# Kernel optimization log

Measured on AMD Instinct MI355X. Metric: run time of the kernel, lower is better.

The kernel has to match this reference:

```python
import jax, jax.numpy as jnp
import numpy as np

N_SUPPORT = 16384
EMBED_DIM = 1024
MAX_LEVELS = 4
N_CLASSES = 64


def setup_inputs() -> dict:
    key = jax.random.key(0)
    ks = jax.random.split(key, 12)
    D, L = EMBED_DIM, MAX_LEVELS
    s = 0.02
    return {
        "support_features": jax.random.normal(ks[0], (N_SUPPORT, D), jnp.float32),
        "support_labels": jax.random.randint(ks[1], (N_SUPPORT,), 0, N_CLASSES),
        "sp_w1": jax.random.normal(ks[2], (D, D // 2), jnp.float32) * s,
        "sp_b1": jnp.zeros((D // 2,), jnp.float32),
        "sp_w2": jax.random.normal(ks[3], (D // 2, L), jnp.float32) * s,
        "sp_b2": jnp.zeros((L,), jnp.float32),
        "lvl_emb": jax.random.normal(ks[4], (L, 1), jnp.float32) * s,
        "an_w1": jax.random.normal(ks[5], (L, D + 1, D), jnp.float32) * s,
        "an_b1": jnp.zeros((L, D), jnp.float32),
        "an_gamma": jnp.ones((L, D), jnp.float32),
        "an_beta": jnp.zeros((L, D), jnp.float32),
        "an_w2": jax.random.normal(ks[6], (L, D, D), jnp.float32) * s,
        "an_b2": jnp.zeros((L, D), jnp.float32),
        "fu_w1": jax.random.normal(ks[7], (L * D + L, D), jnp.float32) * s,
        "fu_b1": jnp.zeros((D,), jnp.float32),
        "fu_w2": jax.random.normal(ks[8], (D, D), jnp.float32) * s,
        "fu_b2": jnp.zeros((D,), jnp.float32),
        "n_classes": N_CLASSES,
    }


def _forward(support_features, support_labels, sp_w1, sp_b1, sp_w2, sp_b2,
             lvl_emb, an_w1, an_b1, an_gamma, an_beta, an_w2, an_b2,
             fu_w1, fu_b1, fu_w2, fu_b2, n_classes):
    N, D = support_features.shape
    L = an_w1.shape[0]
    # structure predictor on task context (mean pooled support set)
    task_context = support_features.mean(axis=0)
    h = jax.nn.relu(task_context @ sp_w1 + sp_b1)
    acts = jax.nn.sigmoid(h @ sp_w2 + sp_b2)  # [L]
    ones = jnp.ones((N,), support_features.dtype)
    counts = jax.ops.segment_sum(ones, support_labels, num_segments=n_classes)[:, None]
    counts = jnp.maximum(counts, 1.0)
    # per-level small MLP over ALL support points, then per-class mean via segment_sum
    protos = []
    for l in range(L):  # fixed small loop over structurally distinct level params
        xl = jnp.concatenate([support_features, jnp.broadcast_to(lvl_emb[l], (N, 1))], axis=1)  # [N, D+1]
        hh = xl @ an_w1[l] + an_b1[l]
        mu = hh.mean(axis=-1, keepdims=True)
        var = ((hh - mu) ** 2).mean(axis=-1, keepdims=True)
        hh = (hh - mu) / jnp.sqrt(var + 1e-5) * an_gamma[l] + an_beta[l]  # LayerNorm eps=1e-5
        hh = jax.nn.relu(hh)
        t = hh @ an_w2[l] + an_b2[l]
        protos.append(jax.ops.segment_sum(t, support_labels, num_segments=n_classes) / counts)
    protos = jnp.stack(protos, axis=1)  # [C, L, D]
    # data-dependent gating: pack prototypes of active levels (act > 0.1) to the front,
    # then active weights, then zero padding -- matching torch's concat+pad layout
    mask = acts > 0.1
    mi = mask.astype(jnp.int32)
    slots = jnp.cumsum(mi) - 1          # destination slot of each active level
    k = mi.sum()                        # number of active levels
    slot_or_dump = jnp.where(mask, slots, L)
    packed = jnp.zeros((n_classes, L + 1, D), protos.dtype).at[:, slot_or_dump, :].set(protos)[:, :L, :]
    S = L * D + L
    buf = jnp.zeros((n_classes, S + 1), protos.dtype)
    buf = buf.at[:, : L * D].set(packed.reshape(n_classes, L * D))
    widx = jnp.where(mask, k * D + slots, S)  # weights placed right after the k packed prototypes
    buf = buf.at[:, widx].set(jnp.broadcast_to(acts, (n_classes, L)))
    fusion_input = buf[:, :S]  # [C, L*D + L]
    fused = jax.nn.relu(fusion_input @ fu_w1 + fu_b1) @ fu_w2 + fu_b2  # [C, D]
    raw_mean = jax.ops.segment_sum(support_features, support_labels, num_segments=n_classes) / counts
    prototypes = jnp.where(k > 0, fused, raw_mean)
    level_contributions = jnp.where(mask, acts, 0.0)
    return prototypes, acts, level_contributions


def reference(support_features, support_labels, sp_w1, sp_b1, sp_w2, sp_b2,
              lvl_emb, an_w1, an_b1, an_gamma, an_beta, an_w2, an_b2,
              fu_w1, fu_b1, fu_w2, fu_b2, n_classes):
    return _forward(support_features, support_labels, sp_w1, sp_b1, sp_w2, sp_b2,
                    lvl_emb, an_w1, an_b1, an_gamma, an_beta, an_w2, an_b2,
                    fu_w1, fu_b1, fu_w2, fu_b2, n_classes)
```

## Files before the change

### kernel.cpp

```cpp
#include <hip/hip_runtime.h>
#include <hip/hip_bf16.h>
#include <stdint.h>

#define N_SUP 16384
#define DIM   1024
#define NLV   4
#define NCLS  64
#define NFUSE 4096

typedef __bf16 bf16x8 __attribute__((ext_vector_type(8)));
typedef __bf16 bf16x4 __attribute__((ext_vector_type(4)));
typedef float  f32x4  __attribute__((ext_vector_type(4)));

#define GLOAD_LDS16(g, l) \
    __builtin_amdgcn_global_load_lds((const __attribute__((address_space(1))) void*)(g), \
                                     (__attribute__((address_space(3))) void*)(l), 16, 0, 0)

__global__ __launch_bounds__(1024) void k_rowlist(const int* __restrict__ labels,
                                                  int* __restrict__ inv,
                                                  int* __restrict__ gstart,
                                                  int* __restrict__ gcnt,
                                                  float* __restrict__ counts_f) {
    __shared__ int cnt[NCLS];
    __shared__ int sstart[NCLS];
    __shared__ int cur[NCLS];
    int tid = threadIdx.x;
    if (tid < NCLS) cnt[tid] = 0;
    __syncthreads();
    for (int r = tid; r < N_SUP; r += 1024) atomicAdd(&cnt[labels[r]], 1);
    __syncthreads();
    if (tid == 0) {
        int run = 0;
        for (int c = 0; c < NCLS; ++c) { sstart[c] = run; run += cnt[c]; }
    }
    __syncthreads();
    if (tid < NCLS) {
        cur[tid] = sstart[tid];
        gstart[tid] = sstart[tid];
        gcnt[tid] = cnt[tid];
        counts_f[tid] = fmaxf((float)cnt[tid], 1.0f);
    }
    __syncthreads();
    for (int r = tid; r < N_SUP; r += 1024) {
        int pos = atomicAdd(&cur[labels[r]], 1);
        inv[r] = pos;
    }
}

__global__ __launch_bounds__(256) void k_conv_feat(const float* __restrict__ f,
                                                   const int* __restrict__ inv,
                                                   __bf16* __restrict__ o) {
    int r = blockIdx.x;
    int tid = threadIdx.x;
    int dr = inv[r];
    float4 v = *(const float4*)(f + (size_t)r * DIM + tid * 4);
    union { __bf16 b[4]; uint64_t u; } pk;
    pk.b[0] = (__bf16)v.x; pk.b[1] = (__bf16)v.y;
    pk.b[2] = (__bf16)v.z; pk.b[3] = (__bf16)v.w;
    *(uint64_t*)(o + (size_t)dr * DIM + tid * 4) = pk.u;
}

__global__ __launch_bounds__(256) void k_wt(const float* __restrict__ an_w1,
                                            __bf16* __restrict__ w1t) {
    __shared__ float tile[64][65];
    int m = blockIdx.z;
    const float* src = an_w1 + (size_t)m * 1025 * 1024;
    __bf16* dst = w1t + (size_t)m * 1024 * 1024;
    int k0 = blockIdx.x * 64, n0 = blockIdx.y * 64;
    int j = threadIdx.x & 63, i0 = threadIdx.x >> 6;
    #pragma unroll
    for (int ii = 0; ii < 16; ++ii) {
        int i = i0 + ii * 4;
        tile[i][j] = src[(size_t)(k0 + i) * 1024 + n0 + j];
    }
    __syncthreads();
    #pragma unroll
    for (int ii = 0; ii < 16; ++ii) {
        int i = i0 + ii * 4;
        dst[(size_t)(n0 + i) * 1024 + k0 + j] = (__bf16)tile[j][i];
    }
}

__global__ __launch_bounds__(256) void k_eff_b1(const float* __restrict__ an_w1,
                                                const float* __restrict__ an_b1,
                                                const float* __restrict__ lvl_emb,
                                                float* __restrict__ eff) {
    int i = blockIdx.x * 256 + threadIdx.x;
    int l = i >> 10, j = i & 1023;
    eff[i] = an_b1[i] + lvl_emb[l] * an_w1[(size_t)l * 1025 * 1024 + (size_t)1024 * 1024 + j];
}

__global__ __launch_bounds__(256) void k_gather(const __bf16* __restrict__ X,
                                                const int* __restrict__ gstart,
                                                const int* __restrict__ gcnt,
                                                float* __restrict__ outp,
                                                float* __restrict__ tcsum) {
    int c = blockIdx.x;
    int col = blockIdx.y * 256 + threadIdx.x;
    int st = gstart[c], n = gcnt[c];
    const __bf16* base = X + (size_t)st * DIM + col;
    float acc = 0.f;
    int i = 0;
    for (; i + 8 <= n; i += 8) {
        float v[8];
        #pragma unroll
        for (int j = 0; j < 8; ++j) v[j] = (float)base[(size_t)(i + j) * DIM];
        #pragma unroll
        for (int j = 0; j < 8; ++j) acc += v[j];
    }
    for (; i < n; ++i) acc += (float)base[(size_t)i * DIM];
    outp[(size_t)c * DIM + col] = acc;
    atomicAdd(&tcsum[col], acc);
}

__global__ __launch_bounds__(512) void k_gemv1(const float* __restrict__ tc,
                                               const float* __restrict__ sp_w1,
                                               float* __restrict__ hpre) {
    __shared__ float tcs[64];
    int tid = threadIdx.x;
    int kb = blockIdx.x * 64;
    if (tid < 64) tcs[tid] = tc[kb + tid] * (1.0f / N_SUP);
    __syncthreads();
    float acc = 0.f;
    #pragma unroll 8
    for (int k = 0; k < 64; ++k)
        acc += tcs[k] * sp_w1[(size_t)(kb + k) * 512 + tid];
    atomicAdd(&hpre[tid], acc);
}

__global__ __launch_bounds__(512) void k_head_fin(const float* __restrict__ hpre,
                                                  const float* __restrict__ sp_b1,
                                                  const float* __restrict__ sp_w2,
                                                  const float* __restrict__ sp_b2,
                                                  float* __restrict__ headf,
                                                  int* __restrict__ headi,
                                                  float* __restrict__ dout) {
    __shared__ float red[512];
    __shared__ float a4[4];
    int tid = threadIdx.x;
    float hv = hpre[tid] + sp_b1[tid];
    hv = hv > 0.f ? hv : 0.f;
    #pragma unroll
    for (int o = 0; o < 4; ++o) {
        red[tid] = hv * sp_w2[tid * 4 + o];
        __syncthreads();
        for (int st = 256; st > 0; st >>= 1) {
            if (tid < st) red[tid] += red[tid + st];
            __syncthreads();
        }
        if (tid == 0) a4[o] = 1.0f / (1.0f + expf(-(red[0] + sp_b2[o])));
        __syncthreads();
    }
    if (tid == 0) {
        int kk = 0;
        int lvl[4] = {-1, -1, -1, -1};
        for (int l = 0; l < 4; ++l)
            if (a4[l] > 0.1f) { lvl[kk] = l; kk++; }
        headi[0] = kk;
        for (int s = 0; s < 4; ++s) headi[1 + s] = lvl[s];
        for (int l = 0; l < 4; ++l) headf[l] = a4[l];
    }
    if (tid < 4) {
        dout[65536 + tid] = a4[tid];
        dout[65540 + tid] = a4[tid] > 0.1f ? a4[tid] : 0.f;
    }
}

__global__ __launch_bounds__(512, 2) void k_gemm256(const __bf16* __restrict__ A,
                                                    const __bf16* __restrict__ Bt,
                                                    const float* __restrict__ bias,
                                                    __bf16* __restrict__ C,
                                                    int K, int Nn, int NT) {
    __shared__ __bf16 lds[65536];
    const int tid = threadIdx.x;
    const int w   = tid >> 6;
    const int l   = tid & 63;
    const int wr  = w >> 2;
    const int wc  = w & 3;
    const int am  = l & 15;
    const int kg  = l >> 4;
    const size_t bm = (size_t)blockIdx.x * 256;
    const size_t bn = (size_t)blockIdx.y * 256;

    const int srow = w * 8 + (l >> 3);
    const int scol = ((l & 7) ^ (l >> 3)) * 8;
    const __bf16* gA[2][2]; const __bf16* gB[2][2];
    #pragma unroll
    for (int h = 0; h < 2; ++h)
        #pragma unroll
        for (int p = 0; p < 2; ++p) {
            gA[h][p] = A  + (bm + h * 128 + p * 64 + srow) * (size_t)K + scol;
            gB[h][p] = Bt + (bn + h * 128 + p * 64 + srow) * (size_t)K + scol;
        }

    f32x4 acc[8][4] = {};
    bf16x8 ax[4][2], ay[4][2], bx[2][2], by[2][2];

    #pragma unroll
    for (int h = 0; h < 2; ++h)
        #pragma unroll
        for (int p = 0; p < 2; ++p) {
            GLOAD_LDS16(gA[h][p], lds + h * 8192 + p * 4096 + w * 512);
            GLOAD_LDS16(gB[h][p], lds + 16384 + h * 8192 + p * 4096 + w * 512);
        }
    asm volatile("s_waitcnt vmcnt(0)" ::: "memory");
    __builtin_amdgcn_s_barrier();

    const int swz = (am & 7) * 8;
    const int ko0 = (kg * 8) ^ swz;
    const int ko1 = (32 + kg * 8) ^ swz;
    {
        const __bf16* pa0 = lds + wr * 8192;
        #pragma unroll
        for (int i = 0; i < 4; ++i) {
            ax[i][0] = *(const bf16x8*)(pa0 + (i * 16 + am) * 64 + ko0);
            ax[i][1] = *(const bf16x8*)(pa0 + (i * 16 + am) * 64 + ko1);
        }
    }

#define MFMAQ(qm, qn, AF, BF) \
    __builtin_amdgcn_s_setprio(1); \
    _Pragma("unroll") \
    for (int i_ = 0; i_ < 4; ++i_) \
        _Pragma("unroll") \
        for (int j_ = 0; j_ < 2; ++j_) \
            _Pragma("unroll") \
            for (int k_ = 0; k_ < 2; ++k_) \
                acc[(qm) * 4 + i_][(qn) * 2 + j_] = __builtin_amdgcn_mfma_f32_16x16x32_bf16( \
                    AF[i_][k_], BF[j_][k_], acc[(qm) * 4 + i_][(qn) * 2 + j_], 0, 0, 0); \
    __builtin_amdgcn_s_setprio(0);

    for (int t = 0; t < NT; ++t) {
        const int cb = (t & 1) * 32768;
        const int nb = cb ^ 32768;
        const int tn = (t + 1) * 64;
        const bool more = (t + 1 < NT);
        const __bf16* pa  = lds + cb + wr * 8192;
        const __bf16* pan = lds + nb + wr * 8192;
        const __bf16* pb  = lds + cb + 16384 + (wc >> 1) * 8192 + (wc & 1) * 4096;

        if (more) {
            GLOAD_LDS16(gA[0][0] + tn, lds + nb + 0 * 4096 + w * 512);
            GLOAD_LDS16(gA[1][0] + tn, lds + nb + 8192 + 0 * 4096 + w * 512);
            asm volatile("s_waitcnt vmcnt(2)" ::: "memory");
        } else {
            asm volatile("s_waitcnt vmcnt(0)" ::: "memory");
        }
        __builtin_amdgcn_s_barrier();
        #pragma unroll
        for (int j = 0; j < 2; ++j) {
            bx[j][0] = *(const bf16x8*)(pb + (j * 16 + am) * 64 + ko0);
            bx[j][1] = *(const bf16x8*)(pb + (j * 16 + am) * 64 + ko1);
        }
        ay[0][0] = *(const bf16x8*)(pa + ((4 + 0) * 16 + am) * 64 + ko0);
        ay[0][1] = *(const bf16x8*)(pa + ((4 + 0) * 16 + am) * 64 + ko1);
        MFMAQ(0, 0, ax, bx)

        if (more) {
            GLOAD_LDS16(gA[0][1] + tn, lds + nb + 1 * 4096 + w * 512);
            GLOAD_LDS16(gA[1][1] + tn, lds + nb + 8192 + 1 * 4096 + w * 512);
        }
        __builtin_amdgcn_s_barrier();
        #pragma unroll
        for (int j = 0; j < 2; ++j) {
            by[j][0] = *(const bf16x8*)(pb + ((2 + j) * 16 + am) * 64 + ko0);
            by[j][1] = *(const bf16x8*)(pb + ((2 + j) * 16 + am) * 64 + ko1);
        }
        ay[1][0] = *(const bf16x8*)(pa + ((4 + 1) * 16 + am) * 64 + ko0);
        ay[1][1] = *(const bf16x8*)(pa + ((4 + 1) * 16 + am) * 64 + ko1);
        MFMAQ(0, 1, ax, by)

        if (more) {
            GLOAD_LDS16(gB[0][0] + tn, lds + nb + 16384 + 0 * 4096 + w * 512);
            GLOAD_LDS16(gB[0][1] + tn, lds + nb + 16384 + 1 * 4096 + w * 512);
            asm volatile("s_waitcnt vmcnt(4)" ::: "memory");
        }
        __builtin_amdgcn_s_barrier();
        #pragma unroll
        for (int i = 2; i < 4; ++i) {
            ay[i][0] = *(const bf16x8*)(pa + ((4 + i) * 16 + am) * 64 + ko0);
            ay[i][1] = *(const bf16x8*)(pa + ((4 + i) * 16 + am) * 64 + ko1);
        }
        if (more) {
            #pragma unroll
            for (int i = 0; i < 2; ++i) {
                ax[i][0] = *(const bf16x8*)(pan + (i * 16 + am) * 64 + ko0);
                ax[i][1] = *(const bf16x8*)(pan + (i * 16 + am) * 64 + ko1);
            }
        }
        MFMAQ(1, 0, ay, bx)

        if (more) {
            GLOAD_LDS16(gB[1][0] + tn, lds + nb + 16384 + 8192 + 0 * 4096 + w * 512);
            GLOAD_LDS16(gB[1][1] + tn, lds + nb + 16384 + 8192 + 1 * 4096 + w * 512);
        }
        __builtin_amdgcn_s_barrier();
        if (more) {
            #pragma unroll
            for (int i = 2; i < 4; ++i) {
                ax[i][0] = *(const bf16x8*)(pan + (i * 16 + am) * 64 + ko0);
                ax[i][1] = *(const bf16x8*)(pan + (i * 16 + am) * 64 + ko1);
            }
        }
        MFMAQ(1, 1, ay, by)
    }
#undef MFMAQ

    const int rbase = kg * 4;
    #pragma unroll
    for (int m = 0; m < 8; ++m) {
        const size_t row = bm + wr * 128 + m * 16 + rbase;
        #pragma unroll
        for (int n = 0; n < 4; ++n) {
            const int col = (int)bn + wc * 64 + n * 16 + am;
            const float bv = bias[col];
            #pragma unroll
            for (int r = 0; r < 4; ++r)
                C[(row + r) * (size_t)Nn + col] = (__bf16)(acc[m][n][r] + bv);
        }
    }
}

__global__ __launch_bounds__(256) void k_gather_ln(const __bf16* __restrict__ hh,
                                                   const float* __restrict__ an_g,
                                                   const float* __restrict__ an_be,
                                                   const int* __restrict__ gstart,
                                                   const int* __restrict__ gcnt,
                                                   float* __restrict__ gsum) {
    int c = blockIdx.x, lv = blockIdx.y, z = blockIdx.z;
    int tid = threadIdx.x;
    int wv = tid >> 6, lane = tid & 63;
    int colb = lane * 16;
    float g[16], b[16];
    #pragma unroll
    for (int j = 0; j < 16; j += 4) {
        float4 gv = *(const float4*)(an_g + lv * 1024 + colb + j);
        float4 bv = *(const float4*)(an_be + lv * 1024 + colb + j);
        g[j] = gv.x; g[j + 1] = gv.y; g[j + 2] = gv.z; g[j + 3] = gv.w;
        b[j] = bv.x; b[j + 1] = bv.y; b[j + 2] = bv.z; b[j + 3] = bv.w;
    }
    int st = gstart[c], n = gcnt[c];
    float acc[16] = {};
    #pragma unroll 2
    for (int i = z * 4 + wv; i < n; i += 8) {
        const __bf16* row = hh + (size_t)(st + i) * NFUSE + lv * 1024 + colb;
        bf16x8 v0 = *(const bf16x8*)row;
        bf16x8 v1 = *(const bf16x8*)(row + 8);
        float x[16];
        #pragma unroll
        for (int j = 0; j < 8; ++j) { x[j] = (float)v0[j]; x[8 + j] = (float)v1[j]; }
        float s = 0.f, q = 0.f;
        #pragma unroll
        for (int j = 0; j < 16; ++j) { s += x[j]; q += x[j] * x[j]; }
        #pragma unroll
        for (int off = 1; off < 64; off <<= 1) {
            s += __shfl_xor(s, off);
            q += __shfl_xor(q, off);
        }
        float mu = s * (1.0f / DIM);
        float var = q * (1.0f / DIM) - mu * mu;
        float rstd = rsqrtf(var + 1e-5f);
        #pragma unroll
        for (int j = 0; j < 16; ++j) {
            float y = (x[j] - mu) * rstd * g[j] + b[j];
            acc[j] += y > 0.f ? y : 0.f;
        }
    }
    __shared__ float red[4][1024];
    #pragma unroll
    for (int j = 0; j < 16; ++j) red[wv][colb + j] = acc[j];
    __syncthreads();
    for (int col = tid; col < 1024; col += 256) {
        float v = red[0][col] + red[1][col] + red[2][col] + red[3][col];
        atomicAdd(&gsum[(size_t)c * NFUSE + lv * 1024 + col], v);
    }
}

__global__ __launch_bounds__(256) void k_build_fi(const float* __restrict__ proto_pre,
                                                  const float* __restrict__ an_b2,
                                                  const int* __restrict__ gcnt,
                                                  const float* __restrict__ counts_f,
                                                  const float* __restrict__ headf,
                                                  const int* __restrict__ headi,
                                                  float* __restrict__ fi) {
    int idx = blockIdx.x * 256 + threadIdx.x;
    if (idx >= 64 * 4160) return;
    int c = idx / 4160, col = idx % 4160;
    int kk = headi[0];
    float v = 0.f;
    if (col < kk * 1024) {
        int s = col >> 10, d = col & 1023;
        int l = headi[1 + s];
        if (gcnt[c] > 0)
            v = proto_pre[((size_t)l * NCLS + c) * DIM + d] / counts_f[c]
                + an_b2[(size_t)l * DIM + d];
    } else if (col < kk * 1024 + kk) {
        int s = col - kk * 1024;
        v = headf[headi[1 + s]];
    }
    fi[idx] = v;
}

__global__ __launch_bounds__(256) void k_fuse_gemm(const float* __restrict__ Abase, int lda, int az,
                                                   const float* __restrict__ Wbase, int wz,
                                                   float* __restrict__ outbase, int oz,
                                                   const float* __restrict__ abias,
                                                   int K) {
    const float* Afi = Abase + (size_t)blockIdx.z * az;
    const float* W   = Wbase + (size_t)blockIdx.z * wz;
    float* outp      = outbase + (size_t)blockIdx.z * oz;
    __shared__ float fi_lds[64][64];
    int tid = threadIdx.x;
    int tj = tid & 63, tg = tid >> 6;
    int jb = blockIdx.x;
    int k0 = blockIdx.y * 64;
    for (int i = tid; i < 64 * 64; i += 256) {
        int cc = i >> 6, kq = i & 63;
        float av = 0.f;
        if (k0 + kq < lda) {
            av = Afi[(size_t)cc * lda + k0 + kq];
            if (abias) {
                av += abias[k0 + kq];
                av = av > 0.f ? av : 0.f;
            }
        }
        fi_lds[cc][kq] = av;
    }
    __syncthreads();
    float acc[16] = {};
    #pragma unroll 4
    for (int kq = 0; kq < 64; ++kq) {
        int kg = k0 + kq;
        float wv = (kg < K) ? W[(size_t)kg * 1024 + jb * 64 + tj] : 0.f;
        #pragma unroll
        for (int cc = 0; cc < 16; ++cc)
            acc[cc] += fi_lds[tg * 16 + cc][kq] * wv;
    }
    #pragma unroll
    for (int cc = 0; cc < 16; ++cc)
        atomicAdd(&outp[(size_t)(tg * 16 + cc) * 1024 + jb * 64 + tj], acc[cc]);
}

__global__ __launch_bounds__(256) void k_final(const float* __restrict__ pre2,
                                               const float* __restrict__ fu_b2,
                                               const int* __restrict__ headi,
                                               const float* __restrict__ rawsum,
                                               const float* __restrict__ counts_f,
                                               float* __restrict__ dout) {
    int i = blockIdx.x * 256 + threadIdx.x;
    int c = i >> 10, j = i & 1023;
    float v;
    if (headi[0] > 0) v = pre2[i] + fu_b2[j];
    else              v = rawsum[i] / counts_f[c];
    dout[i] = v;
}

extern "C" void kernel_launch(void* const* d_in, const int* in_sizes, int n_in,
                              void* d_out, int out_size, void* d_ws, size_t ws_size,
                              hipStream_t stream) {
    (void)in_sizes; (void)n_in; (void)out_size; (void)ws_size;
    const float* feat    = (const float*)d_in[0];
    const int*   labels  = (const int*)d_in[1];
    const float* sp_w1   = (const float*)d_in[2];
    const float* sp_b1   = (const float*)d_in[3];
    const float* sp_w2   = (const float*)d_in[4];
    const float* sp_b2   = (const float*)d_in[5];
    const float* lvl_emb = (const float*)d_in[6];
    const float* an_w1   = (const float*)d_in[7];
    const float* an_b1   = (const float*)d_in[8];
    const float* an_g    = (const float*)d_in[9];
    const float* an_be   = (const float*)d_in[10];
    const float* an_w2   = (const float*)d_in[11];
    const float* an_b2   = (const float*)d_in[12];
    const float* fu_w1   = (const float*)d_in[13];
    const float* fu_b1   = (const float*)d_in[14];
    const float* fu_w2   = (const float*)d_in[15];
    const float* fu_b2   = (const float*)d_in[16];
    float* dout = (float*)d_out;

    char* p = (char*)d_ws;
    auto alloc = [&](size_t b) { char* r = p; p += (b + 255) & ~(size_t)255; return r; };
    __bf16* featb = (__bf16*)alloc((size_t)N_SUP * DIM * 2);
    __bf16* w1t   = (__bf16*)alloc((size_t)NLV * DIM * DIM * 2);
    __bf16* hh    = (__bf16*)alloc((size_t)N_SUP * NFUSE * 2);
    float*  effb1 = (float*) alloc((size_t)NLV * DIM * 4);
    float*  fi    = (float*) alloc((size_t)64 * 4160 * 4);
    float*  rawsum  = (float*)alloc((size_t)NCLS * DIM * 4);
    int*    inv     = (int*)  alloc((size_t)N_SUP * 4);
    int*    gstart  = (int*)  alloc(NCLS * 4);
    int*    gcnt    = (int*)  alloc(NCLS * 4);
    float*  counts_f= (float*)alloc(NCLS * 4);
    float*  headf   = (float*)alloc(4 * 4);
    int*    headi   = (int*)  alloc(8 * 4);
    char* z0 = p;
    float*  tc      = (float*)alloc(DIM * 4);
    float*  gsum    = (float*)alloc((size_t)NCLS * NFUSE * 4);
    float*  proto_pre = (float*)alloc((size_t)NLV * NCLS * DIM * 4);
    float*  h1pre   = (float*)alloc((size_t)NCLS * DIM * 4);
    float*  f2pre   = (float*)alloc((size_t)NCLS * DIM * 4);
    float*  hpre    = (float*)alloc(512 * 4);
    size_t zbytes = (size_t)(p - z0);
    hipMemsetAsync(z0, 0, zbytes, stream);

    k_eff_b1<<<16, 256, 0, stream>>>(an_w1, an_b1, lvl_emb, effb1);
    k_rowlist<<<1, 1024, 0, stream>>>(labels, inv, gstart, gcnt, counts_f);
    k_conv_feat<<<N_SUP, 256, 0, stream>>>(feat, inv, featb);
    k_wt<<<dim3(16, 16, 4), 256, 0, stream>>>(an_w1, w1t);
    k_gather<<<dim3(NCLS, 4), 256, 0, stream>>>(featb, gstart, gcnt, rawsum, tc);
    k_gemv1<<<16, 512, 0, stream>>>(tc, sp_w1, hpre);
    k_head_fin<<<1, 512, 0, stream>>>(hpre, sp_b1, sp_w2, sp_b2, headf, headi, dout);

    k_gemm256<<<dim3(64, 16), 512, 0, stream>>>(featb, w1t, effb1, hh, DIM, NFUSE, DIM / 64);
    k_gather_ln<<<dim3(NCLS, NLV, 2), 256, 0, stream>>>(hh, an_g, an_be, gstart, gcnt, gsum);
    k_fuse_gemm<<<dim3(16, 16, 4), 256, 0, stream>>>(gsum, NFUSE, 1024,
                                                     an_w2, 1024 * 1024,
                                                     proto_pre, NCLS * DIM, nullptr, 1024);

    k_build_fi<<<(64 * 4160) / 256, 256, 0, stream>>>(proto_pre, an_b2, gcnt, counts_f,
                                                      headf, headi, fi);
    k_fuse_gemm<<<dim3(16, 65, 1), 256, 0, stream>>>(fi, 4160, 0, fu_w1, 0,
                                                     h1pre, 0, nullptr, 4100);
    k_fuse_gemm<<<dim3(16, 16, 1), 256, 0, stream>>>(h1pre, 1024, 0, fu_w2, 0,
                                                     f2pre, 0, fu_b1, 1024);
    k_final<<<NCLS * DIM / 256, 256, 0, stream>>>(f2pre, fu_b2, headi, rawsum, counts_f, dout);
}
```

Before: 328.8 us.

## Restructure GEMM main loop into barrier-separated load/compute phases

Reorganizes the 256x256 bf16 MFMA GEMM main loop. The prologue now issues all global-to-LDS loads without a blocking wait. Each iteration waits on partial vmcnt, loads fragments from the current buffer, and brackets every MFMA quadrant with barriers, instead of prefetching next-tile A fragments across iterations. The aim is a simpler, more regular schedule that interleaves next-tile global loads with LDS reads and keeps waves in lockstep, but the extra barriers per iteration and the loss of cross-iteration register prefetch may cost latency.

New measurement: 336.2 us. 1.02x slower.

```diff
diff --git a/kernel.cpp b/kernel.cpp
--- a/kernel.cpp
+++ b/kernel.cpp
@@ -196,27 +196,18 @@
     f32x4 acc[8][4] = {};
     bf16x8 ax[4][2], ay[4][2], bx[2][2], by[2][2];
 
-    #pragma unroll
-    for (int h = 0; h < 2; ++h)
-        #pragma unroll
-        for (int p = 0; p < 2; ++p) {
-            GLOAD_LDS16(gA[h][p], lds + h * 8192 + p * 4096 + w * 512);
-            GLOAD_LDS16(gB[h][p], lds + 16384 + h * 8192 + p * 4096 + w * 512);
-        }
-    asm volatile("s_waitcnt vmcnt(0)" ::: "memory");
-    __builtin_amdgcn_s_barrier();
+    GLOAD_LDS16(gB[0][0], lds + 16384 + 0 * 4096 + w * 512);
+    GLOAD_LDS16(gB[0][1], lds + 16384 + 1 * 4096 + w * 512);
+    GLOAD_LDS16(gB[1][0], lds + 16384 + 8192 + 0 * 4096 + w * 512);
+    GLOAD_LDS16(gB[1][1], lds + 16384 + 8192 + 1 * 4096 + w * 512);
+    GLOAD_LDS16(gA[0][0], lds + 0 * 4096 + w * 512);
+    GLOAD_LDS16(gA[1][0], lds + 8192 + 0 * 4096 + w * 512);
+    GLOAD_LDS16(gA[0][1], lds + 1 * 4096 + w * 512);
+    GLOAD_LDS16(gA[1][1], lds + 8192 + 1 * 4096 + w * 512);
 
     const int swz = (am & 7) * 8;
     const int ko0 = (kg * 8) ^ swz;
     const int ko1 = (32 + kg * 8) ^ swz;
-    {
-        const __bf16* pa0 = lds + wr * 8192;
-        #pragma unroll
-        for (int i = 0; i < 4; ++i) {
-            ax[i][0] = *(const bf16x8*)(pa0 + (i * 16 + am) * 64 + ko0);
-            ax[i][1] = *(const bf16x8*)(pa0 + (i * 16 + am) * 64 + ko1);
-        }
-    }
 
 #define MFMAQ(qm, qn, AF, BF) \
     __builtin_amdgcn_s_setprio(1); \
@@ -235,74 +226,68 @@
         const int nb = cb ^ 32768;
         const int tn = (t + 1) * 64;
         const bool more = (t + 1 < NT);
-        const __bf16* pa  = lds + cb + wr * 8192;
-        const __bf16* pan = lds + nb + wr * 8192;
-        const __bf16* pb  = lds + cb + 16384 + (wc >> 1) * 8192 + (wc & 1) * 4096;
-
+        const __bf16* pa = lds + cb + wr * 8192;
+        const __bf16* pb = lds + cb + 16384 + (wc >> 1) * 8192 + (wc & 1) * 4096;
+
+        asm volatile("s_waitcnt vmcnt(2)" ::: "memory");
+        __builtin_amdgcn_s_barrier();
+        if (more) {
+            GLOAD_LDS16(gB[0][0] + tn, lds + nb + 16384 + 0 * 4096 + w * 512);
+            GLOAD_LDS16(gB[0][1] + tn, lds + nb + 16384 + 1 * 4096 + w * 512);
+        }
+        #pragma unroll
+        for (int i = 0; i < 4; ++i) {
+            ax[i][0] = *(const bf16x8*)(pa + (i * 16 + am) * 64 + ko0);
+            ax[i][1] = *(const bf16x8*)(pa + (i * 16 + am) * 64 + ko1);
+        }
+        #pragma unroll
+        for (int j = 0; j < 2; ++j) {
+            bx[j][0] = *(const bf16x8*)(pb + (j * 16 + am) * 64 + ko0);
+            bx[j][1] = *(const bf16x8*)(pb + (j * 16 + am) * 64 + ko1);
+        }
+        __builtin_amdgcn_s_barrier();
+        MFMAQ(0, 0, ax, bx)
+        __builtin_amdgcn_s_barrier();
+
+        if (more) {
+            GLOAD_LDS16(gB[1][0] + tn, lds + nb + 16384 + 8192 + 0 * 4096 + w * 512);
+            GLOAD_LDS16(gB[1][1] + tn, lds + nb + 16384 + 8192 + 1 * 4096 + w * 512);
+        }
+        #pragma unroll
+        for (int j = 0; j < 2; ++j) {
+            by[j][0] = *(const bf16x8*)(pb + ((2 + j) * 16 + am) * 64 + ko0);
+            by[j][1] = *(const bf16x8*)(pb + ((2 + j) * 16 + am) * 64 + ko1);
+        }
+        __builtin_amdgcn_s_barrier();
+        MFMAQ(0, 1, ax, by)
+        __builtin_amdgcn_s_barrier();
+
+        if (more) {
+            asm volatile("s_waitcnt vmcnt(4)" ::: "memory");
+        } else {
+            asm volatile("s_waitcnt vmcnt(0)" ::: "memory");
+        }
+        __builtin_amdgcn_s_barrier();
         if (more) {
             GLOAD_LDS16(gA[0][0] + tn, lds + nb + 0 * 4096 + w * 512);
             GLOAD_LDS16(gA[1][0] + tn, lds + nb + 8192 + 0 * 4096 + w * 512);
-            asm volatile("s_waitcnt vmcnt(2)" ::: "memory");
-        } else {
-            asm volatile("s_waitcnt vmcnt(0)" ::: "memory");
-        }
-        __builtin_amdgcn_s_barrier();
-        #pragma unroll
-        for (int j = 0; j < 2; ++j) {
-            bx[j][0] = *(const bf16x8*)(pb + (j * 16 + am) * 64 + ko0);
-            bx[j][1] = *(const bf16x8*)(pb + (j * 16 + am) * 64 + ko1);
-        }
-        ay[0][0] = *(const bf16x8*)(pa + ((4 + 0) * 16 + am) * 64 + ko0);
-        ay[0][1] = *(const bf16x8*)(pa + ((4 + 0) * 16 + am) * 64 + ko1);
-        MFMAQ(0, 0, ax, bx)
+        }
+        #pragma unroll
+        for (int i = 0; i < 4; ++i) {
+            ay[i][0] = *(const bf16x8*)(pa + ((4 + i) * 16 + am) * 64 + ko0);
+            ay[i][1] = *(const bf16x8*)(pa + ((4 + i) * 16 + am) * 64 + ko1);
+        }
+        __builtin_amdgcn_s_barrier();
+        MFMAQ(1, 0, ay, bx)
+        __builtin_amdgcn_s_barrier();
 
         if (more) {
             GLOAD_LDS16(gA[0][1] + tn, lds + nb + 1 * 4096 + w * 512);
             GLOAD_LDS16(gA[1][1] + tn, lds + nb + 8192 + 1 * 4096 + w * 512);
         }
         __builtin_amdgcn_s_barrier();
-        #pragma unroll
-        for (int j = 0; j < 2; ++j) {
-            by[j][0] = *(const bf16x8*)(pb + ((2 + j) * 16 + am) * 64 + ko0);
-            by[j][1] = *(const bf16x8*)(pb + ((2 + j) * 16 + am) * 64 + ko1);
-        }
-        ay[1][0] = *(const bf16x8*)(pa + ((4 + 1) * 16 + am) * 64 + ko0);
-        ay[1][1] = *(const bf16x8*)(pa + ((4 + 1) * 16 + am) * 64 + ko1);
-        MFMAQ(0, 1, ax, by)
-
-        if (more) {
-            GLOAD_LDS16(gB[0][0] + tn, lds + nb + 16384 + 0 * 4096 + w * 512);
-            GLOAD_LDS16(gB[0][1] + tn, lds + nb + 16384 + 1 * 4096 + w * 512);
-            asm volatile("s_waitcnt vmcnt(4)" ::: "memory");
-        }
-        __builtin_amdgcn_s_barrier();
-        #pragma unroll
-        for (int i = 2; i < 4; ++i) {
-            ay[i][0] = *(const bf16x8*)(pa + ((4 + i) * 16 + am) * 64 + ko0);
-            ay[i][1] = *(const bf16x8*)(pa + ((4 + i) * 16 + am) * 64 + ko1);
-        }
-        if (more) {
-            #pragma unroll
-            for (int i = 0; i < 2; ++i) {
-                ax[i][0] = *(const bf16x8*)(pan + (i * 16 + am) * 64 + ko0);
-                ax[i][1] = *(const bf16x8*)(pan + (i * 16 + am) * 64 + ko1);
-            }
-        }
-        MFMAQ(1, 0, ay, bx)
-
-        if (more) {
-            GLOAD_LDS16(gB[1][0] + tn, lds + nb + 16384 + 8192 + 0 * 4096 + w * 512);
-            GLOAD_LDS16(gB[1][1] + tn, lds + nb + 16384 + 8192 + 1 * 4096 + w * 512);
-        }
-        __builtin_amdgcn_s_barrier();
-        if (more) {
-            #pragma unroll
-            for (int i = 2; i < 4; ++i) {
-                ax[i][0] = *(const bf16x8*)(pan + (i * 16 + am) * 64 + ko0);
-                ax[i][1] = *(const bf16x8*)(pan + (i * 16 + am) * 64 + ko1);
-            }
-        }
         MFMAQ(1, 1, ay, by)
+        __builtin_amdgcn_s_barrier();
     }
 #undef MFMAQ
 
```

## Stage GEMM epilogue through LDS for 16-byte stores and swizzle block order

Applied to the files above, without the earlier changes.

The GEMM epilogue now writes accumulators into LDS one half-tile at a time, then reads them back row-contiguously so each thread emits 16-byte bf16x8 global stores with vectorized bias loads. This replaces scattered 2-byte stores. Block indices are also remapped with a hard-coded swizzle (64 x-blocks by 16 y-blocks) to improve L2 reuse across concurrently running blocks. The swizzle assumes a specific grid shape and the staging adds barriers, so it fails for other launch shapes.

After: 332.1 us. Within noise of the previous version (+1.0%).

```diff
diff --git a/kernel.cpp b/kernel.cpp
--- a/kernel.cpp
+++ b/kernel.cpp
@@ -179,8 +179,13 @@
     const int wc  = w & 3;
     const int am  = l & 15;
     const int kg  = l >> 4;
-    const size_t bm = (size_t)blockIdx.x * 256;
-    const size_t bn = (size_t)blockIdx.y * 256;
+
+    const int lin = blockIdx.y * 64 + blockIdx.x;
+    const int swz = (lin & 7) * 128 + (lin >> 3);
+    const int bxi = swz >> 4;
+    const int byi = swz & 15;
+    const size_t bm = (size_t)bxi * 256;
+    const size_t bn = (size_t)byi * 256;
 
     const int srow = w * 8 + (l >> 3);
     const int scol = ((l & 7) ^ (l >> 3)) * 8;
@@ -206,9 +211,9 @@
     asm volatile("s_waitcnt vmcnt(0)" ::: "memory");
     __builtin_amdgcn_s_barrier();
 
-    const int swz = (am & 7) * 8;
-    const int ko0 = (kg * 8) ^ swz;
-    const int ko1 = (32 + kg * 8) ^ swz;
+    const int swzr = (am & 7) * 8;
+    const int ko0 = (kg * 8) ^ swzr;
+    const int ko1 = (32 + kg * 8) ^ swzr;
     {
         const __bf16* pa0 = lds + wr * 8192;
         #pragma unroll
@@ -306,17 +311,39 @@
     }
 #undef MFMAQ
 
+    float* fl = (float*)lds;
+    const int ecol = (tid & 31) * 8;
+    float4 bia0 = *(const float4*)(bias + bn + ecol);
+    float4 bia1 = *(const float4*)(bias + bn + ecol + 4);
     const int rbase = kg * 4;
     #pragma unroll
-    for (int m = 0; m < 8; ++m) {
-        const size_t row = bm + wr * 128 + m * 16 + rbase;
-        #pragma unroll
-        for (int n = 0; n < 4; ++n) {
-            const int col = (int)bn + wc * 64 + n * 16 + am;
-            const float bv = bias[col];
+    for (int h = 0; h < 2; ++h) {
+        __syncthreads();
+        if (wr == h) {
             #pragma unroll
-            for (int r = 0; r < 4; ++r)
-                C[(row + r) * (size_t)Nn + col] = (__bf16)(acc[m][n][r] + bv);
+            for (int m = 0; m < 8; ++m) {
+                const int lr = m * 16 + rbase;
+                #pragma unroll
+                for (int n = 0; n < 4; ++n) {
+                    const int cc = wc * 64 + n * 16 + am;
+                    #pragma unroll
+                    for (int r = 0; r < 4; ++r)
+                        fl[(lr + r) * 256 + cc] = acc[m][n][r];
+                }
+            }
+        }
+        __syncthreads();
+        #pragma unroll
+        for (int it = 0; it < 8; ++it) {
+            const int row = (tid >> 5) + it * 16;
+            f32x4 v0 = *(const f32x4*)(fl + row * 256 + ecol);
+            f32x4 v1 = *(const f32x4*)(fl + row * 256 + ecol + 4);
+            bf16x8 ov;
+            ov[0] = (__bf16)(v0[0] + bia0.x); ov[1] = (__bf16)(v0[1] + bia0.y);
+            ov[2] = (__bf16)(v0[2] + bia0.z); ov[3] = (__bf16)(v0[3] + bia0.w);
+            ov[4] = (__bf16)(v1[0] + bia1.x); ov[5] = (__bf16)(v1[1] + bia1.y);
+            ov[6] = (__bf16)(v1[2] + bia1.z); ov[7] = (__bf16)(v1[3] + bia1.w);
+            *(bf16x8*)(C + (bm + h * 128 + row) * (size_t)Nn + bn + ecol) = ov;
         }
     }
 }
```
